# Performance work log

Hardware: AMD Instinct MI355X
Metric: run time of the kernel (lower is better)

The kernel has to match this reference:

```python
import jax, jax.numpy as jnp
import numpy as np

B, S, E, H = 2, 2048, 1024, 16
HD = E // H


def setup_inputs() -> dict:
    key = jax.random.key(0)
    ks = jax.random.split(key, 9)
    s = 1.0 / np.sqrt(E)
    return {
        "x": jax.random.normal(ks[0], (B, S, E), dtype=jnp.float32),
        "wq": jax.random.uniform(ks[1], (E, E), jnp.float32, -s, s),
        "bq": jax.random.uniform(ks[2], (E,), jnp.float32, -s, s),
        "wk": jax.random.uniform(ks[3], (E, E), jnp.float32, -s, s),
        "bk": jax.random.uniform(ks[4], (E,), jnp.float32, -s, s),
        "wv": jax.random.uniform(ks[5], (E, E), jnp.float32, -s, s),
        "bv": jax.random.uniform(ks[6], (E,), jnp.float32, -s, s),
        "wo": jax.random.uniform(ks[7], (E, E), jnp.float32, -s, s),
        "bo": jax.random.uniform(ks[8], (E,), jnp.float32, -s, s),
    }


def reference(x, wq, bq, wk, bk, wv, bv, wo, bo):
    b, s, e = x.shape
    # QKV projections, reshape to [b, h, s, hd]
    def proj(w, bias):
        y = jnp.einsum('bse,ef->bsf', x, w.T) + bias
        return y.reshape(b, s, H, HD).transpose(0, 2, 1, 3)
    q = proj(wq, bq)
    k = proj(wk, bk)
    v = proj(wv, bv)
    score = jnp.einsum('bhqd,bhkd->bhqk', q, k) / jnp.sqrt(jnp.float32(HD))
    # original: exp(x)/sum(exp(x)) + 1e-8  == softmax(x) + 1e-8
    attn = jax.nn.softmax(score, axis=-1) + 1e-8
    out = jnp.einsum('bhqk,bhkd->bhqd', attn, v)
    out = out.transpose(0, 2, 1, 3).reshape(b, s, e)
    return jnp.einsum('bse,ef->bsf', out, wo.T) + bo
```

## Files before the change

kernel.cpp:

```cpp
#include <hip/hip_runtime.h>
#include <hip/hip_bf16.h>
#include <cstdint>

#define SS 2048
#define EE 1024
#define HH 16
#define HDD 64

typedef __attribute__((ext_vector_type(8))) __bf16 bf16x8;
typedef __attribute__((ext_vector_type(4))) float f32x4;

#define MFMA16(a, b, c) __builtin_amdgcn_mfma_f32_16x16x32_bf16((a), (b), (c), 0, 0, 0)

__device__ __forceinline__ unsigned short f2bf(float f) {
    unsigned int u = __builtin_bit_cast(unsigned int, f);
    u += 0x7FFFu + ((u >> 16) & 1u);
    return (unsigned short)(u >> 16);
}

__device__ __forceinline__ void gll16(const unsigned short* g, unsigned short* l) {
    __builtin_amdgcn_global_load_lds(
        (__attribute__((address_space(1))) unsigned int*)g,
        (__attribute__((address_space(3))) unsigned int*)l, 16, 0, 0);
}

__global__ __launch_bounds__(256) void cvt_all(
    const float* __restrict__ x, const float* __restrict__ wq, const float* __restrict__ wk,
    const float* __restrict__ wv, const float* __restrict__ wo,
    unsigned short* __restrict__ xb, unsigned short* __restrict__ wqb, unsigned short* __restrict__ wkb,
    unsigned short* __restrict__ wvb, unsigned short* __restrict__ wob) {
    int idx = blockIdx.x * 256 + threadIdx.x;
    int i4 = idx << 2;
    const float* src;
    unsigned short* dst;
    int off;
    if (i4 < 4194304) { src = x; dst = xb; off = i4; }
    else {
        int w = (i4 - 4194304) >> 20;
        off = (i4 - 4194304) & 1048575;
        if (w == 0) { src = wq; dst = wqb; }
        else if (w == 1) { src = wk; dst = wkb; }
        else if (w == 2) { src = wv; dst = wvb; }
        else { src = wo; dst = wob; }
    }
    float4 v = *(const float4*)&src[off];
    unsigned int p0 = (unsigned int)f2bf(v.x) | ((unsigned int)f2bf(v.y) << 16);
    unsigned int p1 = (unsigned int)f2bf(v.z) | ((unsigned int)f2bf(v.w) << 16);
    uint2 u; u.x = p0; u.y = p1;
    *(uint2*)&dst[off] = u;
}

template <int MODE, int BNT>
__device__ __forceinline__ void gemm_core(
    const unsigned short* __restrict__ A, const unsigned short* __restrict__ W,
    const float* __restrict__ bias, void* __restrict__ out, int bm, int bn) {
    constexpr int JT = BNT / 32;
    __shared__ unsigned short lsA[128 * 32];
    __shared__ unsigned short lsB[BNT * 32];
    const int t = threadIdx.x;
    const int lane = t & 63, l15 = lane & 15, quad = lane >> 4;
    const int wave = t >> 6;
    const int wm = (wave >> 1) * 64, wn = (wave & 1) * (BNT / 2);

    const int cg = ((t & 3) ^ ((t >> 3) & 3)) * 8;
    const unsigned short* ga = A + (size_t)(bm + (t >> 2)) * 1024 + cg;
    const unsigned short* gb = W + (size_t)(bn + (t >> 2)) * 1024 + cg;

    f32x4 acc[4][JT];
    for (int i = 0; i < 4; i++)
        for (int j = 0; j < JT; j++) acc[i][j] = (f32x4){0.f, 0.f, 0.f, 0.f};

    const int swz = (l15 >> 1) & 3;

    for (int k0 = 0; k0 < 1024; k0 += 32) {
        gll16(ga + k0, &lsA[t * 8]);
        gll16(ga + k0 + 64 * 1024, &lsA[2048 + t * 8]);
        gll16(gb + k0, &lsB[t * 8]);
        if (BNT == 128) gll16(gb + k0 + 64 * 1024, &lsB[2048 + t * 8]);
        __syncthreads();
        bf16x8 af[4], bfr[JT];
        for (int i = 0; i < 4; i++)
            af[i] = *(const bf16x8*)&lsA[(wm + i * 16 + l15) * 32 + ((quad ^ swz) * 8)];
        for (int j = 0; j < JT; j++)
            bfr[j] = *(const bf16x8*)&lsB[(wn + j * 16 + l15) * 32 + ((quad ^ swz) * 8)];
        for (int i = 0; i < 4; i++)
            for (int j = 0; j < JT; j++) acc[i][j] = MFMA16(af[i], bfr[j], acc[i][j]);
        __syncthreads();
    }

    for (int j = 0; j < JT; j++) {
        int n = bn + wn + j * 16 + l15;
        float bj = bias[n];
        for (int i = 0; i < 4; i++) {
            int m0 = bm + wm + i * 16 + quad * 4;
            int srow0 = m0 & 2047, bidx = m0 >> 11;
            if (MODE == 3) {
                size_t headb = ((size_t)bidx * HH + (n >> 6)) * (SS * HDD);
                size_t base = headb + (size_t)(srow0 >> 6) * 4096 +
                              (size_t)(((srow0 >> 4) & 3) * 8 + ((n & 63) >> 3)) * 128 + (n & 7);
                for (int rg = 0; rg < 4; rg++)
                    ((unsigned short*)out)[base + (size_t)((srow0 & 15) + rg) * 8] = f2bf(acc[i][j][rg] + bj);
            } else if (MODE == 4) {
                size_t headb = ((size_t)bidx * HH + (n >> 6)) * (SS * HDD);
                size_t addr = headb + (size_t)(srow0 >> 6) * 4096 + (size_t)((n & 63) >> 4) * 1024 +
                              (size_t)(((srow0 >> 5) & 1) * 4 + ((srow0 >> 3) & 3)) * 128 +
                              (size_t)(n & 15) * 8 + (srow0 & 7);
                float v0 = acc[i][j][0] + bj, v1 = acc[i][j][1] + bj;
                float v2 = acc[i][j][2] + bj, v3 = acc[i][j][3] + bj;
                uint2 w;
                w.x = (unsigned int)f2bf(v0) | ((unsigned int)f2bf(v1) << 16);
                w.y = (unsigned int)f2bf(v2) | ((unsigned int)f2bf(v3) << 16);
                *(uint2*)&((unsigned short*)out)[addr] = w;
            } else {
                for (int rg = 0; rg < 4; rg++) {
                    float val = acc[i][j][rg] + bj;
                    int m = m0 + rg;
                    if (MODE == 0) {
                        ((unsigned short*)out)[(((size_t)(m >> 11) * HH + (n >> 6)) * SS + (m & 2047)) * HDD + (n & 63)] = f2bf(val);
                    } else {
                        ((float*)out)[(size_t)m * 1024 + n] = val;
                    }
                }
            }
        }
    }
}

__global__ __launch_bounds__(256) void gemm_qkv(
    const unsigned short* __restrict__ xb,
    const unsigned short* __restrict__ wqb, const unsigned short* __restrict__ wkb,
    const unsigned short* __restrict__ wvb,
    const float* __restrict__ bq, const float* __restrict__ bk, const float* __restrict__ bv,
    unsigned short* qb, unsigned short* kb, unsigned short* vtb) {
    const int blk = blockIdx.x;
    const int u = blk & 7, r = blk >> 3;
    const int by = u + 8 * (r & 3);
    const int rest = r >> 2;
    const int bx = rest & 7, z = rest >> 3;
    if (z == 0)      gemm_core<0, 128>(xb, wqb, bq, qb,  by * 128, bx * 128);
    else if (z == 1) gemm_core<3, 128>(xb, wkb, bk, kb,  by * 128, bx * 128);
    else             gemm_core<4, 128>(xb, wvb, bv, vtb, by * 128, bx * 128);
}

__global__ __launch_bounds__(256) void gemm_out(
    const unsigned short* __restrict__ ob, const unsigned short* __restrict__ wob,
    const float* __restrict__ bo, float* __restrict__ out) {
    const int blk = blockIdx.x;
    const int u = blk & 7, r = blk >> 3;
    const int by = u + 8 * (r & 3);
    const int bx = r >> 2;
    gemm_core<1, 64>(ob, wob, bo, out, by * 128, bx * 64);
}

#define PSTR 72

__global__ __launch_bounds__(256) void attn_fwd(
    const unsigned short* __restrict__ qb, const unsigned short* __restrict__ kb,
    const unsigned short* __restrict__ vtb, unsigned short* __restrict__ ob) {
    __shared__ unsigned short lsP[4 * 32 * PSTR];
    const int t = threadIdx.x, lane = t & 63, l15 = lane & 15, quad = lane >> 4, wave = t >> 6;
    const int blk = blockIdx.x;
    const int u = blk & 7, r = blk >> 3;
    const int bh = u + 8 * (r & 3);
    const int qt = r >> 2;
    const size_t hoff = (size_t)bh * (SS * HDD);
    const float C = 0.125f * 1.44269504088896f;

    bf16x8 qf[2][2];
    const int qrow = qt * 128 + wave * 32;
    for (int i = 0; i < 2; i++)
        for (int ks = 0; ks < 2; ks++) {
            bf16x8 raw = *(const bf16x8*)&qb[hoff + (size_t)(qrow + i * 16 + l15) * HDD + ks * 32 + quad * 8];
            unsigned short tmp[8];
            *(bf16x8*)tmp = raw;
            for (int j = 0; j < 8; j++) {
                float f = __builtin_bit_cast(float, (unsigned int)tmp[j] << 16);
                tmp[j] = f2bf(f * C);
            }
            qf[i][ks] = *(const bf16x8*)tmp;
        }

    unsigned short onesbuf[8];
    for (int j = 0; j < 8; j++) onesbuf[j] = 0x3F80;
    const bf16x8 onesf = *(const bf16x8*)onesbuf;

    f32x4 lacc[2];
    f32x4 o[2][4];
    for (int i = 0; i < 2; i++) {
        lacc[i] = (f32x4){0.f, 0.f, 0.f, 0.f};
        for (int jh = 0; jh < 4; jh++) o[i][jh] = (f32x4){0.f, 0.f, 0.f, 0.f};
    }

    const int foff = quad * 128 + l15 * 8;
    const unsigned short* kp = kb + hoff + foff;
    const unsigned short* vp = vtb + hoff + foff;
    const int pbase = wave * 32 * PSTR;

    bf16x8 ka[4][2], kbuf[4][2];
    for (int j = 0; j < 4; j++)
        for (int ks = 0; ks < 2; ks++)
            ka[j][ks] = *(const bf16x8*)&kp[j * 1024 + ks * 512];

    auto body = [&](bf16x8 (&kc)[4][2], bf16x8 (&kn)[4][2], int kt) {
        const unsigned short* vbase = vp + kt * 4096;
        const unsigned short* knext = kp + ((kt + 1) & 31) * 4096;

        bf16x8 vf[4][2];
        for (int jh = 0; jh < 4; jh++)
            for (int ks = 0; ks < 2; ks++)
                vf[jh][ks] = *(const bf16x8*)&vbase[jh * 1024 + ks * 512];
        for (int j = 0; j < 4; j++)
            for (int ks = 0; ks < 2; ks++)
                kn[j][ks] = *(const bf16x8*)&knext[j * 1024 + ks * 512];

        f32x4 st[4][2];
        for (int j = 0; j < 4; j++)
            for (int i = 0; i < 2; i++) {
                f32x4 z = (f32x4){0.f, 0.f, 0.f, 0.f};
                z = MFMA16(kc[j][0], qf[i][0], z);
                z = MFMA16(kc[j][1], qf[i][1], z);
                st[j][i] = z;
            }

        for (int j = 0; j < 4; j++)
            for (int i = 0; i < 2; i++) {
                float e0 = __builtin_amdgcn_exp2f(st[j][i][0]);
                float e1 = __builtin_amdgcn_exp2f(st[j][i][1]);
                float e2 = __builtin_amdgcn_exp2f(st[j][i][2]);
                float e3 = __builtin_amdgcn_exp2f(st[j][i][3]);
                uint2 w;
                w.x = (__builtin_bit_cast(unsigned int, e0) >> 16) |
                      (__builtin_bit_cast(unsigned int, e1) & 0xFFFF0000u);
                w.y = (__builtin_bit_cast(unsigned int, e2) >> 16) |
                      (__builtin_bit_cast(unsigned int, e3) & 0xFFFF0000u);
                *(uint2*)&lsP[pbase + (i * 16 + l15) * PSTR + j * 16 + quad * 4] = w;
            }

        bf16x8 pf[2][2];
        for (int i = 0; i < 2; i++)
            for (int ks = 0; ks < 2; ks++)
                pf[i][ks] = *(const bf16x8*)&lsP[pbase + (i * 16 + l15) * PSTR + ks * 32 + quad * 8];
        for (int i = 0; i < 2; i++) {
            for (int jh = 0; jh < 4; jh++) {
                o[i][jh] = MFMA16(pf[i][0], vf[jh][0], o[i][jh]);
                o[i][jh] = MFMA16(pf[i][1], vf[jh][1], o[i][jh]);
            }
            lacc[i] = MFMA16(pf[i][0], onesf, lacc[i]);
            lacc[i] = MFMA16(pf[i][1], onesf, lacc[i]);
        }
    };

    for (int kt = 0; kt < 32; kt += 2) {
        body(ka, kbuf, kt);
        body(kbuf, ka, kt + 1);
    }

    const int b = bh >> 4, h = bh & 15;
    for (int i = 0; i < 2; i++)
        for (int rg = 0; rg < 4; rg++) {
            float inv = 1.f / lacc[i][rg];
            int srow = qt * 128 + wave * 32 + i * 16 + quad * 4 + rg;
            size_t rowoff = ((size_t)b * SS + srow) * EE + h * 64;
            for (int jh = 0; jh < 4; jh++)
                ob[rowoff + jh * 16 + l15] = f2bf(o[i][jh][rg] * inv);
        }
}

extern "C" void kernel_launch(void* const* d_in, const int* in_sizes, int n_in,
                              void* d_out, int out_size, void* d_ws, size_t ws_size,
                              hipStream_t stream) {
    const float* x  = (const float*)d_in[0];
    const float* wq = (const float*)d_in[1];
    const float* bq = (const float*)d_in[2];
    const float* wk = (const float*)d_in[3];
    const float* bk = (const float*)d_in[4];
    const float* wv = (const float*)d_in[5];
    const float* bv = (const float*)d_in[6];
    const float* wo = (const float*)d_in[7];
    const float* bo = (const float*)d_in[8];

    char* ws = (char*)d_ws;
    unsigned short* xb  = (unsigned short*)(ws + 0);
    unsigned short* wqb = (unsigned short*)(ws + 8388608);
    unsigned short* wkb = (unsigned short*)(ws + 10485760);
    unsigned short* wvb = (unsigned short*)(ws + 12582912);
    unsigned short* wob = (unsigned short*)(ws + 14680064);
    unsigned short* qb  = (unsigned short*)(ws + 16777216);
    unsigned short* kb  = (unsigned short*)(ws + 25165824);
    unsigned short* vtb = (unsigned short*)(ws + 33554432);
    unsigned short* ob  = xb;

    cvt_all<<<8192, 256, 0, stream>>>(x, wq, wk, wv, wo, xb, wqb, wkb, wvb, wob);
    gemm_qkv<<<768, 256, 0, stream>>>(xb, wqb, wkb, wvb, bq, bk, bv, qb, kb, vtb);
    attn_fwd<<<512, 256, 0, stream>>>(qb, kb, vtb, ob);
    gemm_out<<<512, 256, 0, stream>>>(ob, wob, bo, (float*)d_out);
}
```

Baseline: 215.0 us.

## Stage K/V tiles through double-buffered LDS with async global-to-LDS loads

Result: faster. 201.5 us (-6.3%).

```diff
diff --git a/kernel.cpp b/kernel.cpp
--- a/kernel.cpp
+++ b/kernel.cpp
@@ -157,6 +157,8 @@
 __global__ __launch_bounds__(256) void attn_fwd(
     const unsigned short* __restrict__ qb, const unsigned short* __restrict__ kb,
     const unsigned short* __restrict__ vtb, unsigned short* __restrict__ ob) {
+    __shared__ unsigned short lsK[2][4096];
+    __shared__ unsigned short lsV[2][4096];
     __shared__ unsigned short lsP[4 * 32 * PSTR];
     const int t = threadIdx.x, lane = t & 63, l15 = lane & 15, quad = lane >> 4, wave = t >> 6;
     const int blk = blockIdx.x;
@@ -191,34 +193,40 @@
         for (int jh = 0; jh < 4; jh++) o[i][jh] = (f32x4){0.f, 0.f, 0.f, 0.f};
     }
 
+    const unsigned short* gk = kb + hoff;
+    const unsigned short* gv = vtb + hoff;
+    const int pbase = wave * 32 * PSTR;
     const int foff = quad * 128 + l15 * 8;
-    const unsigned short* kp = kb + hoff + foff;
-    const unsigned short* vp = vtb + hoff + foff;
-    const int pbase = wave * 32 * PSTR;
-
-    bf16x8 ka[4][2], kbuf[4][2];
-    for (int j = 0; j < 4; j++)
-        for (int ks = 0; ks < 2; ks++)
-            ka[j][ks] = *(const bf16x8*)&kp[j * 1024 + ks * 512];
-
-    auto body = [&](bf16x8 (&kc)[4][2], bf16x8 (&kn)[4][2], int kt) {
-        const unsigned short* vbase = vp + kt * 4096;
-        const unsigned short* knext = kp + ((kt + 1) & 31) * 4096;
-
-        bf16x8 vf[4][2];
-        for (int jh = 0; jh < 4; jh++)
-            for (int ks = 0; ks < 2; ks++)
-                vf[jh][ks] = *(const bf16x8*)&vbase[jh * 1024 + ks * 512];
+
+    gll16(gk + t * 8, &lsK[0][t * 8]);
+    gll16(gk + 2048 + t * 8, &lsK[0][2048 + t * 8]);
+    gll16(gv + t * 8, &lsV[0][t * 8]);
+    gll16(gv + 2048 + t * 8, &lsV[0][2048 + t * 8]);
+
+    for (int kt = 0; kt < 32; kt++) {
+        const int cur = kt & 1, nxt = cur ^ 1;
+        __syncthreads();
+
+        if (kt < 31) {
+            const unsigned short* gkn = gk + (kt + 1) * 4096;
+            const unsigned short* gvn = gv + (kt + 1) * 4096;
+            gll16(gkn + t * 8, &lsK[nxt][t * 8]);
+            gll16(gkn + 2048 + t * 8, &lsK[nxt][2048 + t * 8]);
+            gll16(gvn + t * 8, &lsV[nxt][t * 8]);
+            gll16(gvn + 2048 + t * 8, &lsV[nxt][2048 + t * 8]);
+        }
+
+        bf16x8 kfr[4][2];
         for (int j = 0; j < 4; j++)
             for (int ks = 0; ks < 2; ks++)
-                kn[j][ks] = *(const bf16x8*)&knext[j * 1024 + ks * 512];
+                kfr[j][ks] = *(const bf16x8*)&lsK[cur][j * 1024 + ks * 512 + foff];
 
         f32x4 st[4][2];
         for (int j = 0; j < 4; j++)
             for (int i = 0; i < 2; i++) {
                 f32x4 z = (f32x4){0.f, 0.f, 0.f, 0.f};
-                z = MFMA16(kc[j][0], qf[i][0], z);
-                z = MFMA16(kc[j][1], qf[i][1], z);
+                z = MFMA16(kfr[j][0], qf[i][0], z);
+                z = MFMA16(kfr[j][1], qf[i][1], z);
                 st[j][i] = z;
             }
 
@@ -236,10 +244,13 @@
                 *(uint2*)&lsP[pbase + (i * 16 + l15) * PSTR + j * 16 + quad * 4] = w;
             }
 
-        bf16x8 pf[2][2];
+        bf16x8 pf[2][2], vf[4][2];
         for (int i = 0; i < 2; i++)
             for (int ks = 0; ks < 2; ks++)
                 pf[i][ks] = *(const bf16x8*)&lsP[pbase + (i * 16 + l15) * PSTR + ks * 32 + quad * 8];
+        for (int jh = 0; jh < 4; jh++)
+            for (int ks = 0; ks < 2; ks++)
+                vf[jh][ks] = *(const bf16x8*)&lsV[cur][jh * 1024 + ks * 512 + foff];
         for (int i = 0; i < 2; i++) {
             for (int jh = 0; jh < 4; jh++) {
                 o[i][jh] = MFMA16(pf[i][0], vf[jh][0], o[i][jh]);
@@ -248,11 +259,6 @@
             lacc[i] = MFMA16(pf[i][0], onesf, lacc[i]);
             lacc[i] = MFMA16(pf[i][1], onesf, lacc[i]);
         }
-    };
-
-    for (int kt = 0; kt < 32; kt += 2) {
-        body(ka, kbuf, kt);
-        body(kbuf, ka, kt + 1);
     }
 
     const int b = bh >> 4, h = bh & 15;
```
